# Kernel optimization log

Measured on AMD Instinct MI355X. Metric: run time of the kernel, lower is better.

## Reference

```python
import jax, jax.numpy as jnp
import numpy as np

B, C, T, H0, W0 = 4, 512, 4, 63, 63
NUM_IMAGES = 4
CP = C // (NUM_IMAGES * 3)   # 42, compare-branch channels
CC = C // 2                  # 256, attention channels
AGG_IN = C + CP * 3 * NUM_IMAGES  # 1016


def setup_inputs() -> dict:
    key = jax.random.key(0)
    ks = jax.random.split(key, 9)
    w = lambda k, shape: jax.random.normal(k, shape, jnp.float32) * 0.05
    return {
        "x": jax.random.normal(ks[0], (B, C, T, H0, W0), jnp.float32),
        "Wq": w(ks[1], (CC, C)),
        "Wm": w(ks[2], (CC, C)),
        "Wv": w(ks[3], (CC, C)),
        "Wcat": w(ks[4], (CP, C)),
        "Wsub": w(ks[5], (CP, CC)),
        "Wmul": w(ks[6], (CP, CC)),
        "g_cat": jnp.ones((CP,), jnp.float32), "b_cat": jnp.zeros((CP,), jnp.float32),
        "g_sub": jnp.ones((CP,), jnp.float32), "b_sub": jnp.zeros((CP,), jnp.float32),
        "g_mul": jnp.ones((CP,), jnp.float32), "b_mul": jnp.zeros((CP,), jnp.float32),
        "Wagg": w(ks[7], (C, AGG_IN)),
        "g_agg": jnp.ones((C,), jnp.float32), "b_agg": jnp.zeros((C,), jnp.float32),
    }


def _bn(y, g, b):
    # training-mode batch norm over all dims except channel (dim 1)
    m = jnp.mean(y, axis=(0, 2, 3, 4), keepdims=True)
    v = jnp.var(y, axis=(0, 2, 3, 4), keepdims=True)
    return (y - m) * jax.lax.rsqrt(v + 1e-5) * g.reshape(1, -1, 1, 1, 1) + b.reshape(1, -1, 1, 1, 1)


def _forward(x, Wq, Wm, Wv, Wcat, Wsub, Wmul, g_cat, b_cat, g_sub, b_sub,
             g_mul, b_mul, Wagg, g_agg, b_agg):
    # max_pool3d kernel (1,3,3) stride (1,2,2)
    xp = jax.lax.reduce_window(x, -jnp.inf, jax.lax.max,
                               (1, 1, 1, 3, 3), (1, 1, 1, 2, 2), 'VALID')
    Bn, Cn, Tn, Hn, Wn = xp.shape
    cc, hw, thw = Cn // 2, Hn * Wn, Tn * Hn * Wn

    # --- Attend ---
    Q = jnp.einsum('oc,bcthw->bothw', Wq, xp)
    M = jnp.einsum('oc,bcthw->bothw', Wm, xp)
    V = jnp.einsum('oc,bcthw->bothw', Wv, xp)
    scores = jnp.einsum('bcq,bck->bqk', Q.reshape(Bn, cc, thw),
                        M.reshape(Bn, cc, thw)) / np.sqrt(cc).astype(np.float32)
    # softmax over memory pixels within each memory frame
    A = jax.nn.softmax(scores.reshape(Bn, thw, Tn, hw), axis=-1)  # (B, q=t*h*w, Tm, HWm)
    Vf = V.reshape(Bn, cc, Tn, hw).transpose(0, 2, 3, 1)          # (B, Tm, HWm, cc)
    R = jnp.einsum('bqmj,bmjc->bmqc', A, Vf)                      # (B, Tm, THWq, cc)
    R = R.reshape(Bn, Tn, Tn, Hn, Wn, cc).transpose(0, 5, 1, 2, 3, 4)  # (B, cc, Tm, Tq, H, W)

    # --- Compare ---
    Rflat = R.reshape(Bn, cc, Tn * Tn, Hn, Wn)
    Vexp = jnp.broadcast_to(V[:, :, :, None], (Bn, cc, Tn, Tn, Hn, Wn)).reshape(
        Bn, cc, Tn * Tn, Hn, Wn)
    conv = lambda Wk, y: jnp.einsum('oc,bcshw->boshw', Wk, y)
    Ccat = _bn(conv(Wcat, jnp.concatenate([Rflat, Vexp], axis=1)), g_cat, b_cat)
    Csub = _bn(conv(Wsub, Rflat - Vexp), g_sub, b_sub)
    Cmul = _bn(conv(Wmul, Rflat * Vexp), g_mul, b_mul)
    Cfeat = jax.nn.relu(jnp.concatenate([Ccat, Csub, Cmul], axis=1)
                        .reshape(Bn, -1, Tn, Hn, Wn))

    # --- Aggregate ---
    Y = jnp.concatenate([R.mean(axis=3), V, Cfeat], axis=1)  # (B, 1016, T, H, W)
    Z = _bn(jnp.einsum('oc,bcthw->bothw', Wagg, Y), g_agg, b_agg)
    return jax.nn.relu(xp + Z)


def reference(x, Wq, Wm, Wv, Wcat, Wsub, Wmul, g_cat, b_cat, g_sub, b_sub,
              g_mul, b_mul, Wagg, g_agg, b_agg):
    return _forward(x, Wq, Wm, Wv, Wcat, Wsub, Wmul, g_cat, b_cat, g_sub,
                    b_sub, g_mul, b_mul, Wagg, g_agg, b_agg)
```

## Files before the change

kernel.cpp:

```cpp
#include <hip/hip_runtime.h>
#include <math.h>

constexpr int Bb   = 4;
constexpr int Cch  = 512;
constexpr int HW   = 961;
constexpr int THW  = 3844;
constexpr int NCMP = 126;
constexpr int NPIX = Bb * Cch * THW;
constexpr int Hp = 31, Wp = 31, H0c = 63, W0c = 63;
constexpr int VP = 1024;
#define BN_EPS 1e-5f

typedef __attribute__((ext_vector_type(4))) float floatx4;
typedef __attribute__((ext_vector_type(8))) __bf16 bf16x8;
typedef __attribute__((ext_vector_type(8))) unsigned short ushort8;
typedef __attribute__((ext_vector_type(4))) unsigned short ushort4v;

static __device__ __forceinline__ unsigned short f2bf(float x) {
    unsigned int u = __builtin_bit_cast(unsigned int, x);
    u += 0x7fff + ((u >> 16) & 1);
    return (unsigned short)(u >> 16);
}
static __device__ __forceinline__ float bf2f(unsigned short u) {
    return __builtin_bit_cast(float, ((unsigned int)u) << 16);
}

__global__ __launch_bounds__(256) void k_prep_w(
    const float* __restrict__ Wcat, const float* __restrict__ Wsub,
    const float* __restrict__ Wmul, const float* __restrict__ Wagg,
    unsigned short* __restrict__ Wpk, unsigned short* __restrict__ Wab) {
    int idx = blockIdx.x * 256 + threadIdx.x;
    if (idx < 24576) {
        int row = idx >> 9, k = idx & 511;
        Wpk[idx] = (row < 42) ? f2bf(Wcat[row * 512 + k]) : 0;
    } else if (idx < 36864) {
        int i = idx - 24576;
        int row = i >> 8, k = i & 255;
        Wpk[idx] = (row < 42) ? f2bf(Wsub[row * 256 + k]) : 0;
    } else if (idx < 49152) {
        int i = idx - 36864;
        int row = i >> 8, k = i & 255;
        Wpk[idx] = (row < 42) ? f2bf(Wmul[row * 256 + k]) : 0;
    } else if (idx < 49152 + 524288) {
        int i = idx - 49152;
        int row = i >> 10, k = i & 1023;
        Wab[i] = (k < 1016) ? f2bf(Wagg[(size_t)row * 1016 + k]) : 0;
    }
}

__global__ __launch_bounds__(256) void k_pool(const float* __restrict__ x,
                                              float* __restrict__ xp) {
    int idx = blockIdx.x * 256 + threadIdx.x;
    if (idx >= NPIX) return;
    int w = idx % Wp;
    int h = (idx / Wp) % Hp;
    int bct = idx / HW;
    const float* src = x + (size_t)bct * (H0c * W0c) + (2 * h) * W0c + 2 * w;
    float m = -INFINITY;
    #pragma unroll
    for (int i = 0; i < 3; ++i) {
        m = fmaxf(m, src[i * W0c + 0]);
        m = fmaxf(m, src[i * W0c + 1]);
        m = fmaxf(m, src[i * W0c + 2]);
    }
    xp[idx] = m;
}

__global__ __launch_bounds__(256) void k_xpose(const float* __restrict__ xp,
                                               unsigned short* __restrict__ Xh,
                                               unsigned short* __restrict__ Xl) {
    __shared__ float T[64][65];
    const int p0 = blockIdx.x * 64;
    const int c0 = blockIdx.y * 64;
    const int b  = blockIdx.z;
    const int tid = threadIdx.x;
    {
        int px4 = (tid & 15) * 4;
        int cb = tid >> 4;
        #pragma unroll
        for (int i = 0; i < 4; ++i) {
            int c = cb + i * 16;
            int p = p0 + px4;
            const float* src = xp + ((size_t)(b * Cch + c0 + c)) * THW + p;
            float4 v;
            if (p + 3 < THW) {
                v = *(const float4*)src;
            } else {
                v.x = (p     < THW) ? src[0] : 0.f;
                v.y = (p + 1 < THW) ? src[1] : 0.f;
                v.z = (p + 2 < THW) ? src[2] : 0.f;
                v.w = (p + 3 < THW) ? src[3] : 0.f;
            }
            T[c][px4] = v.x; T[c][px4 + 1] = v.y;
            T[c][px4 + 2] = v.z; T[c][px4 + 3] = v.w;
        }
    }
    __syncthreads();
    {
        int px = tid >> 2;
        int cs = (tid & 3) * 16;
        int p = p0 + px;
        if (p < THW) {
            ushort8 hi[2], lo[2];
            #pragma unroll
            for (int j = 0; j < 16; ++j) {
                float v = T[cs + j][px];
                unsigned short h = f2bf(v);
                hi[j >> 3][j & 7] = h;
                lo[j >> 3][j & 7] = f2bf(v - bf2f(h));
            }
            size_t base = ((size_t)b * THW + p) * 512 + c0 + cs;
            *(ushort8*)&Xh[base]     = hi[0];
            *(ushort8*)&Xh[base + 8] = hi[1];
            *(ushort8*)&Xl[base]     = lo[0];
            *(ushort8*)&Xl[base + 8] = lo[1];
        }
    }
}

__global__ __launch_bounds__(256) void k_qmv_mfma(
    const unsigned short* __restrict__ Xh, const unsigned short* __restrict__ Xl,
    const float* __restrict__ Wq, const float* __restrict__ Wm,
    const float* __restrict__ Wv,
    unsigned short* __restrict__ Qbf, unsigned short* __restrict__ Mbf,
    float* __restrict__ Vcl, unsigned short* __restrict__ Vbf) {
    __shared__ unsigned short Whs[128 * 64] __attribute__((aligned(16)));
    __shared__ unsigned short Wls[128 * 64] __attribute__((aligned(16)));
    const int p0  = blockIdx.x * 128;
    const int sel = blockIdx.y >> 1;
    const int ocr = (blockIdx.y & 1) * 128;
    const int b   = blockIdx.z;
    const float* Wbase = ((sel == 0) ? Wq : (sel == 1) ? Wm : Wv) + (size_t)ocr * 512;
    const int tid = threadIdx.x;
    const int wv = tid >> 6, lane = tid & 63;
    const int l15 = lane & 15, quad = lane >> 4;

    floatx4 acc[8][2];
    #pragma unroll
    for (int i = 0; i < 8; ++i)
        #pragma unroll
        for (int h = 0; h < 2; ++h) acc[i][h] = (floatx4){0.f, 0.f, 0.f, 0.f};

    for (int kc = 0; kc < 512; kc += 64) {
        __syncthreads();
        #pragma unroll
        for (int i = 0; i < 4; ++i) {
            int t = i * 256 + tid;
            int row = t >> 3, c8 = t & 7;
            const float* wr = Wbase + (size_t)row * 512 + kc + c8 * 8;
            float v[8];
            *(float4*)&v[0] = *(const float4*)wr;
            *(float4*)&v[4] = *(const float4*)(wr + 4);
            ushort8 hi, lo;
            #pragma unroll
            for (int j = 0; j < 8; ++j) {
                unsigned short h = f2bf(v[j]);
                hi[j] = h;
                lo[j] = f2bf(v[j] - bf2f(h));
            }
            int addr = row * 64 + ((c8 ^ (row & 7)) << 3);
            *(ushort8*)&Whs[addr] = hi;
            *(ushort8*)&Wls[addr] = lo;
        }
        __syncthreads();
        #pragma unroll
        for (int half = 0; half < 2; ++half) {
            int px = p0 + (wv * 2 + half) * 16 + l15;
            int pxc = min(px, THW - 1);
            const unsigned short* xh = Xh + ((size_t)b * THW + pxc) * 512 + kc;
            const unsigned short* xl = Xl + ((size_t)b * THW + pxc) * 512 + kc;
            #pragma unroll
            for (int ks = 0; ks < 2; ++ks) {
                ushort8 bh = *(const ushort8*)&xh[ks * 32 + quad * 8];
                ushort8 bl = *(const ushort8*)&xl[ks * 32 + quad * 8];
                #pragma unroll
                for (int oct = 0; oct < 8; ++oct) {
                    int row = oct * 16 + l15;
                    int ca = row * 64 + (((ks * 4 + quad) ^ (row & 7)) << 3);
                    ushort8 ah = *(const ushort8*)&Whs[ca];
                    ushort8 al = *(const ushort8*)&Wls[ca];
                    acc[oct][half] = __builtin_amdgcn_mfma_f32_16x16x32_bf16(
                        __builtin_bit_cast(bf16x8, ah),
                        __builtin_bit_cast(bf16x8, bh), acc[oct][half], 0, 0, 0);
                    acc[oct][half] = __builtin_amdgcn_mfma_f32_16x16x32_bf16(
                        __builtin_bit_cast(bf16x8, ah),
                        __builtin_bit_cast(bf16x8, bl), acc[oct][half], 0, 0, 0);
                    acc[oct][half] = __builtin_amdgcn_mfma_f32_16x16x32_bf16(
                        __builtin_bit_cast(bf16x8, al),
                        __builtin_bit_cast(bf16x8, bh), acc[oct][half], 0, 0, 0);
                }
            }
        }
    }
    if (sel < 2) {
        unsigned short* outbf = sel ? Mbf : Qbf;
        const float scale = sel ? 1.0f : 0.0625f;
        #pragma unroll
        for (int half = 0; half < 2; ++half) {
            int px = p0 + (wv * 2 + half) * 16 + l15;
            if (px < THW) {
                #pragma unroll
                for (int oct = 0; oct < 8; ++oct) {
                    int ch = ocr + oct * 16 + quad * 4;
                    ushort4v v;
                    #pragma unroll
                    for (int r = 0; r < 4; ++r) v[r] = f2bf(acc[oct][half][r] * scale);
                    *(ushort4v*)&outbf[((size_t)b * THW + px) * 256 + ch] = v;
                }
            }
        }
    } else {
        #pragma unroll
        for (int half = 0; half < 2; ++half) {
            int px = p0 + (wv * 2 + half) * 16 + l15;
            if (px < THW) {
                int m = px / HW;
                int key = px - m * HW;
                size_t vbbase = (size_t)(b * 4 + m) * 256;
                #pragma unroll
                for (int oct = 0; oct < 8; ++oct) {
                    int ch = ocr + oct * 16 + quad * 4;
                    float4 fv = make_float4(acc[oct][half][0], acc[oct][half][1],
                                            acc[oct][half][2], acc[oct][half][3]);
                    *(float4*)&Vcl[((size_t)b * THW + px) * 256 + ch] = fv;
                    #pragma unroll
                    for (int r = 0; r < 4; ++r)
                        Vbf[(vbbase + ch + r) * VP + key] = f2bf(acc[oct][half][r]);
                }
            }
        }
    }
}

__global__ __launch_bounds__(256, 2) void k_attn_mfma(
    const unsigned short* __restrict__ Qbf, const unsigned short* __restrict__ Mbf,
    const unsigned short* __restrict__ Vbf, unsigned short* __restrict__ Rbf) {
    __shared__ unsigned short Qs[16384] __attribute__((aligned(16)));
    __shared__ unsigned short MV[16384] __attribute__((aligned(16)));
    __shared__ unsigned short Ps[4096] __attribute__((aligned(16)));
    __shared__ float stat_mx[4][64];
    __shared__ float stat_sm[4][64];
    __shared__ float alpha_s[64];
    __shared__ float l_s[64];

    const int bm = blockIdx.x;
    const int b = bm >> 2, m = bm & 3;
    const int q0 = blockIdx.y * 64;
    const int tid = threadIdx.x;
    const int wv = tid >> 6, lane = tid & 63;
    const int l15 = lane & 15, quad = lane >> 4;

    const size_t mbase = ((size_t)b * THW + m * HW) * 256;
    const size_t vb = (size_t)bm * 256 * VP;

    #pragma unroll
    for (int it = 0; it < 8; ++it) {
        int v = it * 256 + tid;
        int row = v >> 5, ck = v & 31;
        int q = q0 + row;
        ushort8 val = {0, 0, 0, 0, 0, 0, 0, 0};
        if (q < THW) val = *(const ushort8*)&Qbf[((size_t)b * THW + q) * 256 + ck * 8];
        *(ushort8*)&Qs[row * 256 + ((ck ^ (row & 7)) << 3)] = val;
    }
    ushort8 mpre[8];
    #pragma unroll
    for (int it = 0; it < 8; ++it) {
        int v = it * 256 + tid;
        int key = v >> 5, ck = v & 31;
        mpre[it] = *(const ushort8*)&Mbf[mbase + (size_t)key * 256 + ck * 8];
    }
    floatx4 o[4][4];
    #pragma unroll
    for (int mt = 0; mt < 4; ++mt)
        #pragma unroll
        for (int nt = 0; nt < 4; ++nt) o[mt][nt] = (floatx4){0.f, 0.f, 0.f, 0.f};
    float m_run[4], l_run[4];
    #pragma unroll
    for (int mt = 0; mt < 4; ++mt) { m_run[mt] = -1e30f; l_run[mt] = 0.f; }

    __syncthreads();
    #pragma unroll
    for (int it = 0; it < 8; ++it) {
        int v = it * 256 + tid;
        int key = v >> 5, ck = v & 31;
        *(ushort8*)&MV[key * 256 + ((ck ^ (key & 7)) << 3)] = mpre[it];
    }
    ushort8 vpre[8];
    #pragma unroll
    for (int it = 0; it < 8; ++it) {
        int u = it * 256 + tid;
        int ch = u >> 3, k8 = (u & 7) << 3;
        vpre[it] = *(const ushort8*)&Vbf[vb + (size_t)ch * VP + k8];
    }
    __syncthreads();

    for (int kt = 0; kt < 16; ++kt) {
        const int k0 = kt * 64;
        const int nv = min(64, HW - k0);
        floatx4 sc[4];
        #pragma unroll
        for (int mt = 0; mt < 4; ++mt) sc[mt] = (floatx4){0.f, 0.f, 0.f, 0.f};
        const int mkey = wv * 16 + l15;
        #pragma unroll
        for (int kci = 0; kci < 8; ++kci) {
            ushort8 mf = *(const ushort8*)&MV[mkey * 256 + (((kci * 4 + quad) ^ (mkey & 7)) << 3)];
            #pragma unroll
            for (int mt = 0; mt < 4; ++mt) {
                int qrow = mt * 16 + l15;
                ushort8 qv = *(const ushort8*)&Qs[qrow * 256 + (((kci * 4 + quad) ^ (qrow & 7)) << 3)];
                sc[mt] = __builtin_amdgcn_mfma_f32_16x16x32_bf16(
                    __builtin_bit_cast(bf16x8, mf),
                    __builtin_bit_cast(bf16x8, qv), sc[mt], 0, 0, 0);
            }
        }
        #pragma unroll
        for (int r = 0; r < 4; ++r) {
            if (wv * 16 + quad * 4 + r >= nv) {
                #pragma unroll
                for (int mt = 0; mt < 4; ++mt) sc[mt][r] = -1e30f;
            }
        }
        float mx[4], sm[4];
        #pragma unroll
        for (int mt = 0; mt < 4; ++mt) {
            float v = fmaxf(fmaxf(sc[mt][0], sc[mt][1]), fmaxf(sc[mt][2], sc[mt][3]));
            v = fmaxf(v, __shfl_xor(v, 16));
            v = fmaxf(v, __shfl_xor(v, 32));
            mx[mt] = v;
        }
        #pragma unroll
        for (int mt = 0; mt < 4; ++mt) {
            float s = 0.f;
            #pragma unroll
            for (int r = 0; r < 4; ++r) {
                bool oob = (wv * 16 + quad * 4 + r) >= nv;
                float p = oob ? 0.f : __expf(sc[mt][r] - mx[mt]);
                sc[mt][r] = p;
                s += p;
            }
            s += __shfl_xor(s, 16);
            s += __shfl_xor(s, 32);
            sm[mt] = s;
        }
        if (quad == 0) {
            #pragma unroll
            for (int mt = 0; mt < 4; ++mt) {
                stat_mx[wv][mt * 16 + l15] = mx[mt];
                stat_sm[wv][mt * 16 + l15] = sm[mt];
            }
        }
        __syncthreads();
        float fown[4];
        #pragma unroll
        for (int mt = 0; mt < 4; ++mt) {
            int qrow = mt * 16 + l15;
            float m0 = stat_mx[0][qrow], m1 = stat_mx[1][qrow];
            float m2 = stat_mx[2][qrow], m3 = stat_mx[3][qrow];
            float gmax = fmaxf(fmaxf(m0, m1), fmaxf(m2, m3));
            float mn = fmaxf(m_run[mt], gmax);
            float al = __expf(m_run[mt] - mn);
            float e0 = __expf(m0 - mn), e1 = __expf(m1 - mn);
            float e2 = __expf(m2 - mn), e3 = __expf(m3 - mn);
            l_run[mt] = l_run[mt] * al + stat_sm[0][qrow] * e0 + stat_sm[1][qrow] * e1
                      + stat_sm[2][qrow] * e2 + stat_sm[3][qrow] * e3;
            m_run[mt] = mn;
            fown[mt] = (wv == 0) ? e0 : (wv == 1) ? e1 : (wv == 2) ? e2 : e3;
            if (wv == 0 && quad == 0) alpha_s[qrow] = al;
        }
        #pragma unroll
        for (int mt = 0; mt < 4; ++mt) {
            int qrow = mt * 16 + l15;
            int base = qrow * 64;
            #pragma unroll
            for (int r = 0; r < 4; ++r) {
                int key = wv * 16 + quad * 4 + r;
                Ps[base + (((key >> 3) ^ (qrow & 7)) << 3) + (key & 7)] =
                    f2bf(sc[mt][r] * fown[mt]);
            }
        }
        #pragma unroll
        for (int it = 0; it < 8; ++it) {
            int u = it * 256 + tid;
            int ch = u >> 3, k8 = (u & 7) << 3;
            *(ushort8*)&MV[ch * 64 + (((k8 >> 3) ^ (ch & 7)) << 3)] = vpre[it];
        }
        if (kt < 15) {
            int k0n = k0 + 64;
            int nvn = min(64, HW - k0n);
            #pragma unroll
            for (int it = 0; it < 8; ++it) {
                int v = it * 256 + tid;
                int key = v >> 5, ck = v & 31;
                ushort8 val = {0, 0, 0, 0, 0, 0, 0, 0};
                if (key < nvn)
                    val = *(const ushort8*)&Mbf[mbase + (size_t)(k0n + key) * 256 + ck * 8];
                mpre[it] = val;
            }
        }
        __syncthreads();
        #pragma unroll
        for (int mt = 0; mt < 4; ++mt) {
            float al[4];
            #pragma unroll
            for (int r = 0; r < 4; ++r) al[r] = alpha_s[mt * 16 + quad * 4 + r];
            #pragma unroll
            for (int nt = 0; nt < 4; ++nt)
                #pragma unroll
                for (int r = 0; r < 4; ++r) o[mt][nt][r] *= al[r];
        }
        #pragma unroll
        for (int ks = 0; ks < 2; ++ks) {
            ushort8 af[4];
            #pragma unroll
            for (int mt = 0; mt < 4; ++mt) {
                int row = mt * 16 + l15;
                af[mt] = *(const ushort8*)&Ps[row * 64 + (((ks * 4 + quad) ^ (row & 7)) << 3)];
            }
            #pragma unroll
            for (int nt = 0; nt < 4; ++nt) {
                int ch = wv * 64 + nt * 16 + l15;
                ushort8 bv = *(const ushort8*)&MV[ch * 64 + (((ks * 4 + quad) ^ (ch & 7)) << 3)];
                #pragma unroll
                for (int mt = 0; mt < 4; ++mt)
                    o[mt][nt] = __builtin_amdgcn_mfma_f32_16x16x32_bf16(
                        __builtin_bit_cast(bf16x8, af[mt]),
                        __builtin_bit_cast(bf16x8, bv), o[mt][nt], 0, 0, 0);
            }
        }
        __syncthreads();
        if (kt < 15) {
            #pragma unroll
            for (int it = 0; it < 8; ++it) {
                int v = it * 256 + tid;
                int key = v >> 5, ck = v & 31;
                *(ushort8*)&MV[key * 256 + ((ck ^ (key & 7)) << 3)] = mpre[it];
            }
            #pragma unroll
            for (int it = 0; it < 8; ++it) {
                int u = it * 256 + tid;
                int ch = u >> 3, k8 = (u & 7) << 3;
                vpre[it] = *(const ushort8*)&Vbf[vb + (size_t)ch * VP + k0 + 64 + k8];
            }
        }
        __syncthreads();
    }
    if (wv == 0 && quad == 0) {
        #pragma unroll
        for (int mt = 0; mt < 4; ++mt) l_s[mt * 16 + l15] = l_run[mt];
    }
    __syncthreads();
    #pragma unroll
    for (int mt = 0; mt < 4; ++mt) {
        float invl[4];
        #pragma unroll
        for (int r = 0; r < 4; ++r) invl[r] = 1.f / l_s[mt * 16 + quad * 4 + r];
        #pragma unroll
        for (int nt = 0; nt < 4; ++nt) {
            int ch = wv * 64 + nt * 16 + l15;
            #pragma unroll
            for (int r = 0; r < 4; ++r) {
                int qrow = mt * 16 + quad * 4 + r;
                MV[qrow * 256 + ch] = f2bf(o[mt][nt][r] * invl[r]);
            }
        }
    }
    __syncthreads();
    #pragma unroll
    for (int k = 0; k < 8; ++k) {
        int idx = k * 256 + tid;
        int qrow = idx >> 5, c = idx & 31;
        int q = q0 + qrow;
        if (q < THW) {
            ushort8 v = *(const ushort8*)&MV[qrow * 256 + c * 8];
            __builtin_nontemporal_store(v,
                (ushort8*)&Rbf[((size_t)bm * THW + q) * 256 + c * 8]);
        }
    }
}

__global__ __launch_bounds__(256) void k_cmp(
    const unsigned short* __restrict__ Rbf, const float* __restrict__ Vcl,
    const unsigned short* __restrict__ Wpk, float* __restrict__ Pc) {
    __shared__ unsigned short Ws[24576] __attribute__((aligned(16)));
    const int strip = blockIdx.x;
    const int s = blockIdx.y;
    const int b = blockIdx.z >> 1, kind = blockIdx.z & 1;
    const int m = s >> 2, tq = s & 3;
    const int tid = threadIdx.x;
    const int wv = tid >> 6, lane = tid & 63;
    const int l15 = lane & 15, quad = lane >> 4;

    const unsigned short* wsrc = Wpk + (kind ? 24576 : 0);
    for (int i = tid; i < 3072; i += 256) {
        int row, ch, stride_us;
        if (kind == 0) { row = i >> 6; ch = i & 63; stride_us = 512; }
        else           { row = i >> 5; ch = i & 31; stride_us = 256; }
        ushort8 v = *(const ushort8*)&wsrc[i * 8];
        *(ushort8*)&Ws[row * stride_us + ((ch ^ (row & 7)) << 3)] = v;
    }
    __syncthreads();

    const size_t rbase = ((size_t)(b * 4 + m) * THW + tq * HW) * 256;
    const size_t vbase = ((size_t)b * THW + m * HW) * 256;

    #pragma unroll
    for (int half = 0; half < 2; ++half) {
        int pxt = wv * 2 + half;
        int hw = strip * 128 + pxt * 16 + l15;
        int hwc = min(hw, HW - 1);
        const unsigned short* rrow = Rbf + rbase + (size_t)hwc * 256;
        const float* vrow = Vcl + vbase + (size_t)hwc * 256;
        bf16x8 fr[8], fs[8];
        #pragma unroll
        for (int ks = 0; ks < 8; ++ks) {
            ushort8 r8 = *(const ushort8*)&rrow[ks * 32 + quad * 8];
            float vv[8];
            *(float4*)&vv[0] = *(const float4*)&vrow[ks * 32 + quad * 8];
            *(float4*)&vv[4] = *(const float4*)&vrow[ks * 32 + quad * 8 + 4];
            bf16x8 a, c;
            if (kind == 0) {
                a = __builtin_bit_cast(bf16x8, r8);
                #pragma unroll
                for (int j = 0; j < 8; ++j) c[j] = (__bf16)vv[j];
            } else {
                #pragma unroll
                for (int j = 0; j < 8; ++j) {
                    float rj = bf2f(r8[j]);
                    a[j] = (__bf16)(rj - vv[j]);
                    c[j] = (__bf16)(rj * vv[j]);
                }
            }
            fr[ks] = a; fs[ks] = c;
        }
        floatx4 acc[6];
        #pragma unroll
        for (int i = 0; i < 6; ++i) acc[i] = (floatx4){0.f, 0.f, 0.f, 0.f};
        if (kind == 0) {
            #pragma unroll
            for (int ks = 0; ks < 16; ++ks) {
                bf16x8 bfr = (ks < 8) ? fr[ks] : fs[ks - 8];
                #pragma unroll
                for (int cit = 0; cit < 3; ++cit) {
                    int row = cit * 16 + l15;
                    ushort8 aw = *(const ushort8*)&Ws[row * 512 + (((ks * 4 + quad) ^ (row & 7)) << 3)];
                    acc[cit] = __builtin_amdgcn_mfma_f32_16x16x32_bf16(
                        __builtin_bit_cast(bf16x8, aw), bfr, acc[cit], 0, 0, 0);
                }
            }
        } else {
            #pragma unroll
            for (int ks = 0; ks < 8; ++ks) {
                #pragma unroll
                for (int cit = 0; cit < 6; ++cit) {
                    int row = cit * 16 + l15;
                    ushort8 aw = *(const ushort8*)&Ws[row * 256 + (((ks * 4 + quad) ^ (row & 7)) << 3)];
                    bf16x8 bfr = (cit < 3) ? fr[ks] : fs[ks];
                    acc[cit] = __builtin_amdgcn_mfma_f32_16x16x32_bf16(
                        __builtin_bit_cast(bf16x8, aw), bfr, acc[cit], 0, 0, 0);
                }
            }
        }
        if (hw < HW) {
            if (kind == 0) {
                #pragma unroll
                for (int cit = 0; cit < 3; ++cit)
                    #pragma unroll
                    for (int r = 0; r < 4; ++r) {
                        int ci = cit * 16 + quad * 4 + r;
                        if (ci < 42)
                            Pc[((size_t)(b * NCMP + ci) * 16 + s) * HW + hw] = acc[cit][r];
                    }
            } else {
                #pragma unroll
                for (int cit = 0; cit < 6; ++cit)
                    #pragma unroll
                    for (int r = 0; r < 4; ++r) {
                        int cl = (cit % 3) * 16 + quad * 4 + r;
                        if (cl < 42) {
                            int ci = (cit < 3 ? 42 : 84) + cl;
                            Pc[((size_t)(b * NCMP + ci) * 16 + s) * HW + hw] = acc[cit][r];
                        }
                    }
            }
        }
    }
}

__global__ __launch_bounds__(256) void k_stats_cmp(
    const float* __restrict__ Pc, const float* __restrict__ g_cat,
    const float* __restrict__ b_cat, const float* __restrict__ g_sub,
    const float* __restrict__ b_sub, const float* __restrict__ g_mul,
    const float* __restrict__ b_mul, float* __restrict__ bnc) {
    const int c = blockIdx.x, tid = threadIdx.x;
    float s = 0.f, q = 0.f;
    for (int i = tid; i < 4 * 16 * HW; i += 256) {
        int bb = i / (16 * HW), r = i - bb * (16 * HW);
        float v = Pc[(size_t)(bb * NCMP + c) * (16 * HW) + r];
        s += v; q += v * v;
    }
    __shared__ float rs[256], rq[256];
    rs[tid] = s; rq[tid] = q;
    __syncthreads();
    for (int off = 128; off > 0; off >>= 1) {
        if (tid < off) { rs[tid] += rs[tid + off]; rq[tid] += rq[tid + off]; }
        __syncthreads();
    }
    if (tid == 0) {
        const float n = 4.f * 16.f * HW;
        float mean = rs[0] / n;
        float var = rq[0] / n - mean * mean;
        float g, bt;
        if (c < 42)       { g = g_cat[c];      bt = b_cat[c]; }
        else if (c < 84)  { g = g_sub[c - 42]; bt = b_sub[c - 42]; }
        else              { g = g_mul[c - 84]; bt = b_mul[c - 84]; }
        float sc = g * rsqrtf(var + BN_EPS);
        bnc[c] = sc;
        bnc[NCMP + c] = bt - mean * sc;
    }
}

__global__ __launch_bounds__(256) void k_build_y(
    const unsigned short* __restrict__ Rbf, const float* __restrict__ Vcl,
    const float* __restrict__ Pc, const float* __restrict__ bnc,
    unsigned short* __restrict__ Ybf) {
    const int strip = blockIdx.x, t = blockIdx.y, b = blockIdx.z;
    const int tid = threadIdx.x;
    const int chl = tid & 31;
    const int hwl = tid >> 5;
    for (int pass = 0; pass < 8; ++pass) {
        int hw = strip * 64 + pass * 8 + hwl;
        if (hw >= HW) continue;
        size_t ybase = ((size_t)b * THW + t * HW + hw) * 1024;
        for (int cb = 0; cb < 8; ++cb) {
            int ch = cb * 128 + chl * 4;
            float v[4];
            if (ch < 256) {
                v[0] = v[1] = v[2] = v[3] = 0.f;
                #pragma unroll
                for (int tq = 0; tq < 4; ++tq) {
                    ushort4v rv = *(const ushort4v*)&Rbf[
                        (((size_t)(b * 4 + t)) * THW + tq * HW + hw) * 256 + ch];
                    v[0] += bf2f(rv[0]); v[1] += bf2f(rv[1]);
                    v[2] += bf2f(rv[2]); v[3] += bf2f(rv[3]);
                }
                v[0] *= 0.25f; v[1] *= 0.25f; v[2] *= 0.25f; v[3] *= 0.25f;
            } else if (ch < 512) {
                float4 vv = *(const float4*)&Vcl[((size_t)b * THW + t * HW + hw) * 256 + (ch - 256)];
                v[0] = vv.x; v[1] = vv.y; v[2] = vv.z; v[3] = vv.w;
            } else if (ch < 1016) {
                int ci = (ch - 512) >> 2;
                float sc = bnc[ci], sh = bnc[NCMP + ci];
                #pragma unroll
                for (int mm = 0; mm < 4; ++mm) {
                    float pv = Pc[(((size_t)(b * NCMP + ci)) * 16 + mm * 4 + t) * HW + hw];
                    v[mm] = fmaxf(fmaf(pv, sc, sh), 0.f);
                }
            } else {
                v[0] = v[1] = v[2] = v[3] = 0.f;
            }
            ushort4v ov;
            #pragma unroll
            for (int i = 0; i < 4; ++i) ov[i] = f2bf(v[i]);
            *(ushort4v*)&Ybf[ybase + ch] = ov;
        }
    }
}

__global__ __launch_bounds__(256) void k_aggm(
    const unsigned short* __restrict__ Wab, const unsigned short* __restrict__ Ybf,
    float* __restrict__ Z) {
    __shared__ unsigned short Wt[16384] __attribute__((aligned(16)));
    const int p0 = blockIdx.x * 128;
    const int oc0 = blockIdx.y * 128;
    const int b = blockIdx.z;
    const int tid = threadIdx.x;
    const int wv = tid >> 6, lane = tid & 63;
    const int l15 = lane & 15, quad = lane >> 4;
    floatx4 acc[8][2];
    #pragma unroll
    for (int i = 0; i < 8; ++i)
        #pragma unroll
        for (int h = 0; h < 2; ++h) acc[i][h] = (floatx4){0.f, 0.f, 0.f, 0.f};
    for (int kc = 0; kc < 8; ++kc) {
        __syncthreads();
        for (int i = tid; i < 2048; i += 256) {
            int row = i >> 4, ch = i & 15;
            ushort8 v = *(const ushort8*)&Wab[(size_t)(oc0 + row) * 1024 + kc * 128 + ch * 8];
            *(ushort8*)&Wt[row * 128 + ((ch ^ (row & 7)) << 3)] = v;
        }
        __syncthreads();
        #pragma unroll
        for (int half = 0; half < 2; ++half) {
            int px = p0 + (wv * 2 + half) * 16 + l15;
            int pxc = min(px, THW - 1);
            const unsigned short* yrow = Ybf + ((size_t)b * THW + pxc) * 1024 + kc * 128;
            #pragma unroll
            for (int ks = 0; ks < 4; ++ks) {
                ushort8 bf = *(const ushort8*)&yrow[ks * 32 + quad * 8];
                #pragma unroll
                for (int oct = 0; oct < 8; ++oct) {
                    int row = oct * 16 + l15;
                    ushort8 af = *(const ushort8*)&Wt[row * 128 + ((((ks * 4 + quad) ^ (row & 7))) << 3)];
                    acc[oct][half] = __builtin_amdgcn_mfma_f32_16x16x32_bf16(
                        __builtin_bit_cast(bf16x8, af),
                        __builtin_bit_cast(bf16x8, bf), acc[oct][half], 0, 0, 0);
                }
            }
        }
    }
    #pragma unroll
    for (int half = 0; half < 2; ++half) {
        int px = p0 + (wv * 2 + half) * 16 + l15;
        if (px < THW) {
            #pragma unroll
            for (int oct = 0; oct < 8; ++oct) {
                int oc = oc0 + oct * 16 + quad * 4;
                #pragma unroll
                for (int r = 0; r < 4; ++r)
                    Z[((size_t)(b * Cch + oc + r)) * THW + px] = acc[oct][half][r];
            }
        }
    }
}

__global__ __launch_bounds__(256) void k_stats_agg(
    const float* __restrict__ Z, const float* __restrict__ g_agg,
    const float* __restrict__ b_agg, float* __restrict__ bna) {
    const int c = blockIdx.x, tid = threadIdx.x;
    float s = 0.f, q = 0.f;
    for (int i = tid; i < 4 * THW; i += 256) {
        int bb = i / THW, p = i - bb * THW;
        float v = Z[((size_t)bb * Cch + c) * THW + p];
        s += v; q += v * v;
    }
    __shared__ float rs[256], rq[256];
    rs[tid] = s; rq[tid] = q;
    __syncthreads();
    for (int off = 128; off > 0; off >>= 1) {
        if (tid < off) { rs[tid] += rs[tid + off]; rq[tid] += rq[tid + off]; }
        __syncthreads();
    }
    if (tid == 0) {
        const float n = 4.f * THW;
        float mean = rs[0] / n;
        float var = rq[0] / n - mean * mean;
        float sc = g_agg[c] * rsqrtf(var + BN_EPS);
        bna[c] = sc;
        bna[Cch + c] = b_agg[c] - mean * sc;
    }
}

__global__ __launch_bounds__(256) void k_final(const float* __restrict__ xp,
                                               const float* __restrict__ Z,
                                               const float* __restrict__ bna,
                                               float* __restrict__ out) {
    int idx = blockIdx.x * 256 + threadIdx.x;
    if (idx >= NPIX) return;
    int c = (idx / THW) & 511;
    out[idx] = fmaxf(fmaf(Z[idx], bna[c], bna[Cch + c]) + xp[idx], 0.f);
}

extern "C" void kernel_launch(void* const* d_in, const int* in_sizes, int n_in,
                              void* d_out, int out_size, void* d_ws, size_t ws_size,
                              hipStream_t stream) {
    const float* x     = (const float*)d_in[0];
    const float* Wq    = (const float*)d_in[1];
    const float* Wm    = (const float*)d_in[2];
    const float* Wv    = (const float*)d_in[3];
    const float* Wcat  = (const float*)d_in[4];
    const float* Wsub  = (const float*)d_in[5];
    const float* Wmul  = (const float*)d_in[6];
    const float* g_cat = (const float*)d_in[7];
    const float* b_cat = (const float*)d_in[8];
    const float* g_sub = (const float*)d_in[9];
    const float* b_sub = (const float*)d_in[10];
    const float* g_mul = (const float*)d_in[11];
    const float* b_mul = (const float*)d_in[12];
    const float* Wagg  = (const float*)d_in[13];
    const float* g_agg = (const float*)d_in[14];
    const float* b_agg = (const float*)d_in[15];
    float* out = (float*)d_out;
    float* ws  = (float*)d_ws;

    float* xp  = ws;
    float* Vcl = xp + 7872512;
    float* bnc = Vcl + 3936256;
    float* bna = bnc + 512;
    unsigned short* Wpk = (unsigned short*)(bna + 1024);
    unsigned short* Wab = Wpk + 49152;
    float* bfreg = (float*)(Wab + 524288);
    unsigned short* Qbf = (unsigned short*)bfreg;
    unsigned short* Mbf = Qbf + 3936256;
    unsigned short* Vbf = Mbf + 3936256;
    unsigned short* Ybf = (unsigned short*)bfreg;
    unsigned short* Rbf = (unsigned short*)(bfreg + 7872512);
    float* Pc = (float*)(Rbf + 15745024);
    float* Z  = (float*)Rbf;
    unsigned short* Xh = Rbf;
    unsigned short* Xl = Xh + 7872512;

    k_prep_w<<<dim3(2240), dim3(256), 0, stream>>>(Wcat, Wsub, Wmul, Wagg, Wpk, Wab);
    k_pool<<<dim3((NPIX + 255) / 256), dim3(256), 0, stream>>>(x, xp);
    k_xpose<<<dim3(61, 8, Bb), dim3(256), 0, stream>>>(xp, Xh, Xl);
    k_qmv_mfma<<<dim3(31, 6, Bb), dim3(256), 0, stream>>>(Xh, Xl, Wq, Wm, Wv,
                                                          Qbf, Mbf, Vcl, Vbf);
    k_attn_mfma<<<dim3(16, 61), dim3(256), 0, stream>>>(Qbf, Mbf, Vbf, Rbf);
    k_cmp<<<dim3(8, 16, 8), dim3(256), 0, stream>>>(Rbf, Vcl, Wpk, Pc);
    k_stats_cmp<<<dim3(NCMP), dim3(256), 0, stream>>>(Pc, g_cat, b_cat, g_sub, b_sub,
                                                      g_mul, b_mul, bnc);
    k_build_y<<<dim3(16, 4, Bb), dim3(256), 0, stream>>>(Rbf, Vcl, Pc, bnc, Ybf);
    k_aggm<<<dim3(31, 4, Bb), dim3(256), 0, stream>>>(Wab, Ybf, Z);
    k_stats_agg<<<dim3(Cch), dim3(256), 0, stream>>>(Z, g_agg, b_agg, bna);
    k_final<<<dim3((NPIX + 255) / 256), dim3(256), 0, stream>>>(xp, Z, bna, out);
}
```

Measured before the change: 678.1 us.

## Restructure attention kernel: per-wave query rows, register Q, direct-to-LDS K/V loads

The attention kernel now gives each wave its own 16 query rows, with Q held in registers. Every wave scores all 64 keys of a tile, so the online-softmax max and sum reduce inside the wave instead of through the cross-wave statistics arrays in shared memory. M and V tiles share one LDS buffer and are loaded with global_load_lds straight into swizzled LDS, which removes the register staging and cuts LDS use so launch bounds can allow 3 blocks per CU. The V tail padding columns are now zeroed in the weight-prep kernel, because the V loads no longer mask out-of-range keys. The single buffer adds more barriers per tile and leaves less room to overlap loads with compute.

```diff
diff --git a/kernel.cpp b/kernel.cpp
--- a/kernel.cpp
+++ b/kernel.cpp
@@ -25,10 +25,18 @@
     return __builtin_bit_cast(float, ((unsigned int)u) << 16);
 }
 
+static __device__ __forceinline__ void gl_lds16(const unsigned short* g,
+                                                unsigned short* l) {
+    __builtin_amdgcn_global_load_lds(
+        (const __attribute__((address_space(1))) void*)g,
+        (__attribute__((address_space(3))) void*)l, 16, 0, 0);
+}
+
 __global__ __launch_bounds__(256) void k_prep_w(
     const float* __restrict__ Wcat, const float* __restrict__ Wsub,
     const float* __restrict__ Wmul, const float* __restrict__ Wagg,
-    unsigned short* __restrict__ Wpk, unsigned short* __restrict__ Wab) {
+    unsigned short* __restrict__ Wpk, unsigned short* __restrict__ Wab,
+    unsigned short* __restrict__ Vbf) {
     int idx = blockIdx.x * 256 + threadIdx.x;
     if (idx < 24576) {
         int row = idx >> 9, k = idx & 511;
@@ -45,6 +53,10 @@
         int i = idx - 49152;
         int row = i >> 10, k = i & 1023;
         Wab[i] = (k < 1016) ? f2bf(Wagg[(size_t)row * 1016 + k]) : 0;
+    } else if (idx < 573440 + 258048) {
+        int i = idx - 573440;
+        int row = i / 63, k = i - row * 63;
+        Vbf[(size_t)row * VP + 961 + k] = 0;
     }
 }
 
@@ -232,14 +244,11 @@
     }
 }
 
-__global__ __launch_bounds__(256, 2) void k_attn_mfma(
+__global__ __launch_bounds__(256, 3) void k_attn_mfma(
     const unsigned short* __restrict__ Qbf, const unsigned short* __restrict__ Mbf,
     const unsigned short* __restrict__ Vbf, unsigned short* __restrict__ Rbf) {
-    __shared__ unsigned short Qs[16384] __attribute__((aligned(16)));
-    __shared__ unsigned short MV[16384] __attribute__((aligned(16)));
+    __shared__ unsigned short KV[16384] __attribute__((aligned(16)));
     __shared__ unsigned short Ps[4096] __attribute__((aligned(16)));
-    __shared__ float stat_mx[4][64];
-    __shared__ float stat_sm[4][64];
     __shared__ float alpha_s[64];
     __shared__ float l_s[64];
 
@@ -249,49 +258,34 @@
     const int tid = threadIdx.x;
     const int wv = tid >> 6, lane = tid & 63;
     const int l15 = lane & 15, quad = lane >> 4;
+    const int x7 = l15 & 7;
 
     const size_t mbase = ((size_t)b * THW + m * HW) * 256;
     const size_t vb = (size_t)bm * 256 * VP;
 
-    #pragma unroll
-    for (int it = 0; it < 8; ++it) {
-        int v = it * 256 + tid;
-        int row = v >> 5, ck = v & 31;
-        int q = q0 + row;
-        ushort8 val = {0, 0, 0, 0, 0, 0, 0, 0};
-        if (q < THW) val = *(const ushort8*)&Qbf[((size_t)b * THW + q) * 256 + ck * 8];
-        *(ushort8*)&Qs[row * 256 + ((ck ^ (row & 7)) << 3)] = val;
-    }
-    ushort8 mpre[8];
-    #pragma unroll
-    for (int it = 0; it < 8; ++it) {
-        int v = it * 256 + tid;
-        int key = v >> 5, ck = v & 31;
-        mpre[it] = *(const ushort8*)&Mbf[mbase + (size_t)key * 256 + ck * 8];
-    }
+    const int qg = min(q0 + wv * 16 + l15, THW - 1);
+    const unsigned short* qp = Qbf + ((size_t)b * THW + qg) * 256 + quad * 8;
+    ushort8 qreg[8];
+    #pragma unroll
+    for (int kci = 0; kci < 8; ++kci)
+        qreg[kci] = *(const ushort8*)&qp[kci * 32];
+
+    #pragma unroll
+    for (int i = 0; i < 8; ++i) {
+        int blk = wv * 8 + i;
+        int key = blk * 2 + (lane >> 5);
+        int cS = (lane & 31) ^ (key & 7);
+        int kg = min(key, HW - 1);
+        gl_lds16(Mbf + mbase + (size_t)kg * 256 + (cS << 3), &KV[blk * 512]);
+    }
+
     floatx4 o[4][4];
     #pragma unroll
     for (int mt = 0; mt < 4; ++mt)
         #pragma unroll
         for (int nt = 0; nt < 4; ++nt) o[mt][nt] = (floatx4){0.f, 0.f, 0.f, 0.f};
-    float m_run[4], l_run[4];
-    #pragma unroll
-    for (int mt = 0; mt < 4; ++mt) { m_run[mt] = -1e30f; l_run[mt] = 0.f; }
-
-    __syncthreads();
-    #pragma unroll
-    for (int it = 0; it < 8; ++it) {
-        int v = it * 256 + tid;
-        int key = v >> 5, ck = v & 31;
-        *(ushort8*)&MV[key * 256 + ((ck ^ (key & 7)) << 3)] = mpre[it];
-    }
-    ushort8 vpre[8];
-    #pragma unroll
-    for (int it = 0; it < 8; ++it) {
-        int u = it * 256 + tid;
-        int ch = u >> 3, k8 = (u & 7) << 3;
-        vpre[it] = *(const ushort8*)&Vbf[vb + (size_t)ch * VP + k8];
-    }
+    float m_run = -1e30f, l_run = 0.f;
+
     __syncthreads();
 
     for (int kt = 0; kt < 16; ++kt) {
@@ -299,127 +293,91 @@
         const int nv = min(64, HW - k0);
         floatx4 sc[4];
         #pragma unroll
-        for (int mt = 0; mt < 4; ++mt) sc[mt] = (floatx4){0.f, 0.f, 0.f, 0.f};
-        const int mkey = wv * 16 + l15;
-        #pragma unroll
-        for (int kci = 0; kci < 8; ++kci) {
-            ushort8 mf = *(const ushort8*)&MV[mkey * 256 + (((kci * 4 + quad) ^ (mkey & 7)) << 3)];
-            #pragma unroll
-            for (int mt = 0; mt < 4; ++mt) {
-                int qrow = mt * 16 + l15;
-                ushort8 qv = *(const ushort8*)&Qs[qrow * 256 + (((kci * 4 + quad) ^ (qrow & 7)) << 3)];
-                sc[mt] = __builtin_amdgcn_mfma_f32_16x16x32_bf16(
+        for (int kb = 0; kb < 4; ++kb) sc[kb] = (floatx4){0.f, 0.f, 0.f, 0.f};
+        #pragma unroll
+        for (int kb = 0; kb < 4; ++kb) {
+            const int key = kb * 16 + l15;
+            #pragma unroll
+            for (int kci = 0; kci < 8; ++kci) {
+                ushort8 mf = *(const ushort8*)&KV[key * 256 +
+                    ((((kci << 2) + quad) ^ x7) << 3)];
+                sc[kb] = __builtin_amdgcn_mfma_f32_16x16x32_bf16(
                     __builtin_bit_cast(bf16x8, mf),
-                    __builtin_bit_cast(bf16x8, qv), sc[mt], 0, 0, 0);
-            }
-        }
-        #pragma unroll
-        for (int r = 0; r < 4; ++r) {
-            if (wv * 16 + quad * 4 + r >= nv) {
-                #pragma unroll
-                for (int mt = 0; mt < 4; ++mt) sc[mt][r] = -1e30f;
-            }
-        }
-        float mx[4], sm[4];
+                    __builtin_bit_cast(bf16x8, qreg[kci]), sc[kb], 0, 0, 0);
+            }
+        }
+        __syncthreads();
+        #pragma unroll
+        for (int i = 0; i < 8; ++i) {
+            int blk = wv * 8 + i;
+            int ch = blk * 8 + (lane >> 3);
+            int cS = (lane & 7) ^ (ch & 7);
+            gl_lds16(Vbf + vb + (size_t)ch * VP + k0 + (cS << 3), &KV[blk * 512]);
+        }
+        #pragma unroll
+        for (int kb = 0; kb < 4; ++kb) {
+            #pragma unroll
+            for (int r = 0; r < 4; ++r)
+                if (kb * 16 + quad * 4 + r >= nv) sc[kb][r] = -1e30f;
+        }
+        float mx = -1e30f;
+        #pragma unroll
+        for (int kb = 0; kb < 4; ++kb)
+            mx = fmaxf(mx, fmaxf(fmaxf(sc[kb][0], sc[kb][1]),
+                                 fmaxf(sc[kb][2], sc[kb][3])));
+        mx = fmaxf(mx, __shfl_xor(mx, 16));
+        mx = fmaxf(mx, __shfl_xor(mx, 32));
+        float m_new = fmaxf(m_run, mx);
+        float al = __expf(m_run - m_new);
+        float sm = 0.f;
+        #pragma unroll
+        for (int kb = 0; kb < 4; ++kb) {
+            #pragma unroll
+            for (int r = 0; r < 4; ++r) {
+                float p = __expf(sc[kb][r] - m_new);
+                sc[kb][r] = p;
+                sm += p;
+            }
+        }
+        sm += __shfl_xor(sm, 16);
+        sm += __shfl_xor(sm, 32);
+        l_run = l_run * al + sm;
+        m_run = m_new;
+        if (quad == 0) alpha_s[wv * 16 + l15] = al;
+        {
+            const int prow = wv * 16 + l15;
+            #pragma unroll
+            for (int kb = 0; kb < 4; ++kb) {
+                ushort4v pk;
+                #pragma unroll
+                for (int r = 0; r < 4; ++r) pk[r] = f2bf(sc[kb][r]);
+                int cW = ((kb << 1) + (quad >> 1)) ^ x7;
+                *(ushort4v*)&Ps[prow * 64 + (cW << 3) + ((quad & 1) << 2)] = pk;
+            }
+        }
+        __syncthreads();
         #pragma unroll
         for (int mt = 0; mt < 4; ++mt) {
-            float v = fmaxf(fmaxf(sc[mt][0], sc[mt][1]), fmaxf(sc[mt][2], sc[mt][3]));
-            v = fmaxf(v, __shfl_xor(v, 16));
-            v = fmaxf(v, __shfl_xor(v, 32));
-            mx[mt] = v;
-        }
-        #pragma unroll
-        for (int mt = 0; mt < 4; ++mt) {
-            float s = 0.f;
-            #pragma unroll
-            for (int r = 0; r < 4; ++r) {
-                bool oob = (wv * 16 + quad * 4 + r) >= nv;
-                float p = oob ? 0.f : __expf(sc[mt][r] - mx[mt]);
-                sc[mt][r] = p;
-                s += p;
-            }
-            s += __shfl_xor(s, 16);
-            s += __shfl_xor(s, 32);
-            sm[mt] = s;
-        }
-        if (quad == 0) {
-            #pragma unroll
-            for (int mt = 0; mt < 4; ++mt) {
-                stat_mx[wv][mt * 16 + l15] = mx[mt];
-                stat_sm[wv][mt * 16 + l15] = sm[mt];
-            }
-        }
-        __syncthreads();
-        float fown[4];
-        #pragma unroll
-        for (int mt = 0; mt < 4; ++mt) {
-            int qrow = mt * 16 + l15;
-            float m0 = stat_mx[0][qrow], m1 = stat_mx[1][qrow];
-            float m2 = stat_mx[2][qrow], m3 = stat_mx[3][qrow];
-            float gmax = fmaxf(fmaxf(m0, m1), fmaxf(m2, m3));
-            float mn = fmaxf(m_run[mt], gmax);
-            float al = __expf(m_run[mt] - mn);
-            float e0 = __expf(m0 - mn), e1 = __expf(m1 - mn);
-            float e2 = __expf(m2 - mn), e3 = __expf(m3 - mn);
-            l_run[mt] = l_run[mt] * al + stat_sm[0][qrow] * e0 + stat_sm[1][qrow] * e1
-                      + stat_sm[2][qrow] * e2 + stat_sm[3][qrow] * e3;
-            m_run[mt] = mn;
-            fown[mt] = (wv == 0) ? e0 : (wv == 1) ? e1 : (wv == 2) ? e2 : e3;
-            if (wv == 0 && quad == 0) alpha_s[qrow] = al;
-        }
-        #pragma unroll
-        for (int mt = 0; mt < 4; ++mt) {
-            int qrow = mt * 16 + l15;
-            int base = qrow * 64;
-            #pragma unroll
-            for (int r = 0; r < 4; ++r) {
-                int key = wv * 16 + quad * 4 + r;
-                Ps[base + (((key >> 3) ^ (qrow & 7)) << 3) + (key & 7)] =
-                    f2bf(sc[mt][r] * fown[mt]);
-            }
-        }
-        #pragma unroll
-        for (int it = 0; it < 8; ++it) {
-            int u = it * 256 + tid;
-            int ch = u >> 3, k8 = (u & 7) << 3;
-            *(ushort8*)&MV[ch * 64 + (((k8 >> 3) ^ (ch & 7)) << 3)] = vpre[it];
-        }
-        if (kt < 15) {
-            int k0n = k0 + 64;
-            int nvn = min(64, HW - k0n);
-            #pragma unroll
-            for (int it = 0; it < 8; ++it) {
-                int v = it * 256 + tid;
-                int key = v >> 5, ck = v & 31;
-                ushort8 val = {0, 0, 0, 0, 0, 0, 0, 0};
-                if (key < nvn)
-                    val = *(const ushort8*)&Mbf[mbase + (size_t)(k0n + key) * 256 + ck * 8];
-                mpre[it] = val;
-            }
-        }
-        __syncthreads();
-        #pragma unroll
-        for (int mt = 0; mt < 4; ++mt) {
-            float al[4];
-            #pragma unroll
-            for (int r = 0; r < 4; ++r) al[r] = alpha_s[mt * 16 + quad * 4 + r];
+            float alq[4];
+            #pragma unroll
+            for (int r = 0; r < 4; ++r) alq[r] = alpha_s[mt * 16 + quad * 4 + r];
             #pragma unroll
             for (int nt = 0; nt < 4; ++nt)
                 #pragma unroll
-                for (int r = 0; r < 4; ++r) o[mt][nt][r] *= al[r];
+                for (int r = 0; r < 4; ++r) o[mt][nt][r] *= alq[r];
         }
         #pragma unroll
         for (int ks = 0; ks < 2; ++ks) {
             ushort8 af[4];
             #pragma unroll
-            for (int mt = 0; mt < 4; ++mt) {
-                int row = mt * 16 + l15;
-                af[mt] = *(const ushort8*)&Ps[row * 64 + (((ks * 4 + quad) ^ (row & 7)) << 3)];
-            }
+            for (int mt = 0; mt < 4; ++mt)
+                af[mt] = *(const ushort8*)&Ps[(mt * 16 + l15) * 64 +
+                    ((((ks << 2) + quad) ^ x7) << 3)];
             #pragma unroll
             for (int nt = 0; nt < 4; ++nt) {
                 int ch = wv * 64 + nt * 16 + l15;
-                ushort8 bv = *(const ushort8*)&MV[ch * 64 + (((ks * 4 + quad) ^ (ch & 7)) << 3)];
+                ushort8 bv = *(const ushort8*)&KV[ch * 64 +
+                    ((((ks << 2) + quad) ^ x7) << 3)];
                 #pragma unroll
                 for (int mt = 0; mt < 4; ++mt)
                     o[mt][nt] = __builtin_amdgcn_mfma_f32_16x16x32_bf16(
@@ -429,25 +387,19 @@
         }
         __syncthreads();
         if (kt < 15) {
-            #pragma unroll
-            for (int it = 0; it < 8; ++it) {
-                int v = it * 256 + tid;
-                int key = v >> 5, ck = v & 31;
-                *(ushort8*)&MV[key * 256 + ((ck ^ (key & 7)) << 3)] = mpre[it];
-            }
-            #pragma unroll
-            for (int it = 0; it < 8; ++it) {
-                int u = it * 256 + tid;
-                int ch = u >> 3, k8 = (u & 7) << 3;
-                vpre[it] = *(const ushort8*)&Vbf[vb + (size_t)ch * VP + k0 + 64 + k8];
-            }
-        }
-        __syncthreads();
-    }
-    if (wv == 0 && quad == 0) {
-        #pragma unroll
-        for (int mt = 0; mt < 4; ++mt) l_s[mt * 16 + l15] = l_run[mt];
-    }
+            int k0n = k0 + 64;
+            #pragma unroll
+            for (int i = 0; i < 8; ++i) {
+                int blk = wv * 8 + i;
+                int key = blk * 2 + (lane >> 5);
+                int cS = (lane & 31) ^ (key & 7);
+                int kg = min(k0n + key, HW - 1);
+                gl_lds16(Mbf + mbase + (size_t)kg * 256 + (cS << 3), &KV[blk * 512]);
+            }
+        }
+        __syncthreads();
+    }
+    if (quad == 0) l_s[wv * 16 + l15] = l_run;
     __syncthreads();
     #pragma unroll
     for (int mt = 0; mt < 4; ++mt) {
@@ -460,7 +412,7 @@
             #pragma unroll
             for (int r = 0; r < 4; ++r) {
                 int qrow = mt * 16 + quad * 4 + r;
-                MV[qrow * 256 + ch] = f2bf(o[mt][nt][r] * invl[r]);
+                KV[qrow * 256 + ch] = f2bf(o[mt][nt][r] * invl[r]);
             }
         }
     }
@@ -471,7 +423,7 @@
         int qrow = idx >> 5, c = idx & 31;
         int q = q0 + qrow;
         if (q < THW) {
-            ushort8 v = *(const ushort8*)&MV[qrow * 256 + c * 8];
+            ushort8 v = *(const ushort8*)&KV[qrow * 256 + c * 8];
             __builtin_nontemporal_store(v,
                 (ushort8*)&Rbf[((size_t)bm * THW + q) * 256 + c * 8]);
         }
@@ -799,7 +751,7 @@
     unsigned short* Xh = Rbf;
     unsigned short* Xl = Xh + 7872512;
 
-    k_prep_w<<<dim3(2240), dim3(256), 0, stream>>>(Wcat, Wsub, Wmul, Wagg, Wpk, Wab);
+    k_prep_w<<<dim3(3248), dim3(256), 0, stream>>>(Wcat, Wsub, Wmul, Wagg, Wpk, Wab, Vbf);
     k_pool<<<dim3((NPIX + 255) / 256), dim3(256), 0, stream>>>(x, xp);
     k_xpose<<<dim3(61, 8, Bb), dim3(256), 0, stream>>>(xp, Xh, Xl);
     k_qmv_mfma<<<dim3(31, 6, Bb), dim3(256), 0, stream>>>(Xh, Xl, Wq, Wm, Wv,
```

Result: slower. 821.6 us (+21.2%).
